# Kernel optimization log

Hardware: AMD Instinct MI355X
Metric: run time of the kernel (lower is better)

Reference implementation:

```python
import jax, jax.numpy as jnp
import numpy as np

L, B, S, D, H = 6, 2, 2048, 512, 8
DH = D // H
FF = 4 * D
EPS = 1e-5


def setup_inputs() -> dict:
    key = jax.random.key(0)
    ks = jax.random.split(key, 10)
    w = lambda k, shape: jax.random.normal(k, shape, jnp.float32) * 0.02
    return {
        "query": jax.random.normal(ks[0], (B, S, D), jnp.float32),
        "key": jax.random.normal(ks[1], (B, S, D), jnp.float32),
        "query_mask": jnp.ones((B, S), jnp.int32),
        "key_mask": jnp.ones((B, S), jnp.int32),
        # per-layer stacked params; conv1d(kernel=1) == linear with weight [out,in]
        "Wq": w(ks[2], (L, D, D)), "bq": jnp.zeros((L, D), jnp.float32),
        "Wk": w(ks[3], (L, D, D)), "bk": jnp.zeros((L, D), jnp.float32),
        "Wv": w(ks[4], (L, D, D)), "bv": jnp.zeros((L, D), jnp.float32),
        "Wo": w(ks[5], (L, D, D)), "bo": jnp.zeros((L, D), jnp.float32),
        "ln1_g": jnp.ones((L, D), jnp.float32), "ln1_b": jnp.zeros((L, D), jnp.float32),
        "ff_w1": w(ks[6], (L, FF, D)), "ff_b1": jnp.zeros((L, FF), jnp.float32),
        "ff_w2": w(ks[7], (L, D, FF)), "ff_b2": jnp.zeros((L, D), jnp.float32),
        "ln2_g": jnp.ones((L, D), jnp.float32), "ln2_b": jnp.zeros((L, D), jnp.float32),
    }


def _layer_norm(x, g, b):
    m = jnp.mean(x, axis=-1, keepdims=True)
    v = jnp.mean(jnp.square(x - m), axis=-1, keepdims=True)
    return (x - m) * jax.lax.rsqrt(v + EPS) * g + b


def reference(query, key, query_mask, key_mask,
              Wq, bq, Wk, bk, Wv, bv, Wo, bo,
              ln1_g, ln1_b, ff_w1, ff_b1, ff_w2, ff_b2, ln2_g, ln2_b):
    b_, s_, d_ = query.shape
    kpad = (key_mask == 0)[:, None, None, :]          # [B,1,1,K]
    qm = query_mask.astype(query.dtype)[:, :, None]    # [B,S,1]
    x = query
    for i in range(L):
        # QKV projections (conv1d kernel-size-1 == linear), split heads -> [B,H,S,DH]
        def split(t):
            return t.reshape(b_, s_, H, DH).transpose(0, 2, 1, 3)
        q = split(x @ Wq[i].T + bq[i]) * (float(DH) ** -0.5)
        k = split(key @ Wk[i].T + bk[i])
        v = split(key @ Wv[i].T + bv[i])
        attn = jnp.einsum('bhqd,bhkd->bhqk', q, k)
        attn = jnp.where(kpad, -jnp.inf, attn)
        attn = jax.nn.softmax(attn, axis=-1)
        o = jnp.einsum('bhqk,bhkd->bhqd', attn, v)
        o = o.transpose(0, 2, 1, 3).reshape(b_, s_, H * DH)
        o = (o @ Wo[i].T + bo[i]) * qm                 # output proj + query mask
        x = _layer_norm(o + x, ln1_g[i], ln1_b[i])
        h = jax.nn.leaky_relu(x @ ff_w1[i].T + ff_b1[i], 0.01)
        f = (h @ ff_w2[i].T + ff_b2[i]) * qm           # FFN mask on output
        x = _layer_norm(f + x, ln2_g[i], ln2_b[i])
    return x
```

## Files before the change

### kernel.cpp

```cpp
#include <hip/hip_runtime.h>
#include <stdint.h>

constexpr int LAYERS = 6;
constexpr int Bc = 2, Sc = 2048, Dc = 512, Hc = 8, DHc = 64, FFc = 2048;
constexpr int Mc = Bc * Sc;
constexpr int NS = 2;
constexpr int KCHUNK = Sc / NS;

typedef __attribute__((ext_vector_type(8))) __bf16 bf16x8;
typedef __attribute__((ext_vector_type(4))) __bf16 bf16x4;
typedef __attribute__((ext_vector_type(4))) float f32x4;

__device__ __forceinline__ void async_ld16(const void* g, void* lds) {
  __builtin_amdgcn_global_load_lds(
      (const __attribute__((address_space(1))) uint32_t*)g,
      (__attribute__((address_space(3))) uint32_t*)lds, 16, 0, 0);
}

__global__ __launch_bounds__(256) void cvt_kernel(const float* __restrict__ in,
                                                  __bf16* __restrict__ out, int n) {
  int i = (blockIdx.x * 256 + threadIdx.x) * 4;
  if (i + 4 > n) return;
  const float4 v = *(const float4*)(in + i);
  bf16x4 o;
  o[0] = (__bf16)v.x; o[1] = (__bf16)v.y; o[2] = (__bf16)v.z; o[3] = (__bf16)v.w;
  *(bf16x4*)(out + i) = o;
}

template <int BM, int BN, int WM, int WN, int EPI>
__global__ __launch_bounds__(256) void gemm_bt(
    const __bf16* __restrict__ A, const __bf16* __restrict__ W,
    const float* __restrict__ bias, const float* __restrict__ bias2,
    float* __restrict__ outf, __bf16* __restrict__ outb,
    __bf16* __restrict__ outb2, float scale,
    int M, int N, int K, int Kstride) {
  constexpr int BK = 32;
  __shared__ __bf16 As[2][BM * BK];
  __shared__ __bf16 Bs[2][BN * BK];
  const int tid = threadIdx.x;
  const int l15 = tid & 15;
  const int lg = (tid & 63) >> 4;
  const int w = tid >> 6;
  const int wm = w >> 1, wn = w & 1;
  const int tm = blockIdx.y * BM;
  const int tn = blockIdx.x * BN;
  const int z = blockIdx.z;
  const __bf16* Ap = A + (size_t)tm * Kstride + (size_t)z * K;
  const __bf16* Wp = W + (size_t)tn * Kstride + (size_t)z * K;
  f32x4 acc[WM][WN] = {};

  auto stage = [&](int k0, int bf) {
#pragma unroll
    for (int c = 0; c < BM * 4 / 256; ++c) {
      int cc = c * 256 + tid;
      async_ld16(Ap + (size_t)(cc >> 2) * Kstride + k0 + (cc & 3) * 8, &As[bf][cc * 8]);
    }
#pragma unroll
    for (int c = 0; c < BN * 4 / 256; ++c) {
      int cc = c * 256 + tid;
      async_ld16(Wp + (size_t)(cc >> 2) * Kstride + k0 + (cc & 3) * 8, &Bs[bf][cc * 8]);
    }
  };

  const int nk = K / BK;
  stage(0, 0);
  __syncthreads();
  int buf = 0;
  for (int t = 0; t < nk; ++t) {
    if (t + 1 < nk) stage((t + 1) * BK, buf ^ 1);
    bf16x8 af[WM], bfr[WN];
#pragma unroll
    for (int i = 0; i < WM; ++i)
      af[i] = *(const bf16x8*)&As[buf][(wm * WM * 16 + i * 16 + l15) * BK + lg * 8];
#pragma unroll
    for (int j = 0; j < WN; ++j)
      bfr[j] = *(const bf16x8*)&Bs[buf][(wn * WN * 16 + j * 16 + l15) * BK + lg * 8];
#pragma unroll
    for (int i = 0; i < WM; ++i)
#pragma unroll
      for (int j = 0; j < WN; ++j)
        acc[i][j] = __builtin_amdgcn_mfma_f32_16x16x32_bf16(af[i], bfr[j], acc[i][j], 0, 0, 0);
    __syncthreads();
    buf ^= 1;
  }

#pragma unroll
  for (int i = 0; i < WM; ++i) {
#pragma unroll
    for (int j = 0; j < WN; ++j) {
      const int n = tn + wn * WN * 16 + j * 16 + l15;
      float bv;
      if constexpr (EPI == 6) {
        int lyr = n >> 10, w1 = n & 1023, p = w1 >> 9, d = w1 & 511;
        bv = (p ? bias2 : bias)[lyr * 512 + d];
      } else if constexpr (EPI == 0) {
        bv = (z == 0) ? bias[n] : 0.f;
      } else {
        bv = bias[n];
      }
#pragma unroll
      for (int r = 0; r < 4; ++r) {
        const int m = tm + wm * WM * 16 + i * 16 + lg * 4 + r;
        float v = acc[i][j][r] + bv;
        if constexpr (EPI == 0) {
          outf[(size_t)z * M * N + (size_t)m * N + n] = v;
        } else if constexpr (EPI == 1) {
          int b = m >> 11, s = m & (Sc - 1);
          int h = n >> 6, dh = n & 63;
          outb[(((size_t)(b * Hc + h)) * Sc + s) * DHc + dh] = (__bf16)(v * scale);
        } else if constexpr (EPI == 4) {
          float lv = v > 0.f ? v : 0.01f * v;
          outb[(size_t)m * N + n] = (__bf16)lv;
        } else if constexpr (EPI == 6) {
          int b = m >> 11, s = m & (Sc - 1);
          int lyr = n >> 10, w1 = n & 1023, p = w1 >> 9, d = w1 & 511;
          int h = d >> 6, dh = d & 63;
          if (p == 0)
            outb[((((size_t)(lyr * Bc + b) * Hc + h)) * Sc + s) * DHc + dh] = (__bf16)v;
          else
            outb2[((((size_t)(lyr * Bc + b) * Hc + h)) * DHc + dh) * Sc + s] = (__bf16)v;
        }
      }
    }
  }
}

__global__ __launch_bounds__(256, 4) void attn_kernel(
    const __bf16* __restrict__ q, const __bf16* __restrict__ k,
    const __bf16* __restrict__ vt, const int* __restrict__ kmask,
    __bf16* __restrict__ Opart, float* __restrict__ mpart,
    float* __restrict__ lpart) {
  const int bh = blockIdx.y;
  const int b = bh >> 3;
  const int z = blockIdx.z;
  const int w = threadIdx.x >> 6;
  const int l = threadIdx.x & 63;
  const int l15 = l & 15;
  const int lg = l >> 4;
  const int tid = threadIdx.x;
  const int qbase = blockIdx.x * 64 + w * 16;
  const int k0 = z * KCHUNK;

  const __bf16* qp = q + ((size_t)bh * Sc + qbase) * DHc;
  const __bf16* kp = k + (size_t)bh * Sc * DHc;
  const __bf16* vp = vt + (size_t)bh * DHc * Sc;

  bf16x8 qf[2];
  qf[0] = *(const bf16x8*)(qp + l15 * DHc + lg * 8);
  qf[1] = *(const bf16x8*)(qp + l15 * DHc + 32 + lg * 8);

  bf16x8 onesf;
#pragma unroll
  for (int i = 0; i < 8; ++i) onesf[i] = (__bf16)1.0f;

  f32x4 oacc[4] = {};
  f32x4 lacc = {};
  float mr[4] = {-1e30f, -1e30f, -1e30f, -1e30f};

  __shared__ __bf16 Ks[2][4096];
  __shared__ __bf16 Vs[2][4096];
  __shared__ __bf16 P[4][1024];

  auto stage = [&](int t, int bf) {
    const int kt = k0 + t * 64;
#pragma unroll
    for (int ii = 0; ii < 2; ++ii) {
      int i = ii * 256 + tid;
      int r = i >> 3;
      int bsrc = (i & 7) ^ (r & 7);
      async_ld16(kp + (size_t)(kt + r) * DHc + bsrc * 8, &Ks[bf][i * 8]);
      async_ld16(vp + (size_t)r * Sc + kt + bsrc * 8, &Vs[bf][i * 8]);
    }
  };

  stage(0, 0);
  __syncthreads();

  constexpr int NT = KCHUNK / 64;
  int buf = 0;
  for (int t = 0; t < NT; ++t) {
    const int kt = k0 + t * 64;
    if (t + 1 < NT) stage(t + 1, buf ^ 1);

    f32x4 sacc[4] = {};
#pragma unroll
    for (int kf = 0; kf < 2; ++kf) {
#pragma unroll
      for (int cb = 0; cb < 4; ++cb) {
        int row = cb * 16 + l15;
        bf16x8 kfr = *(const bf16x8*)&Ks[buf][row * 64 + (((kf * 4 + lg) ^ (row & 7)) * 8)];
        sacc[cb] = __builtin_amdgcn_mfma_f32_16x16x32_bf16(qf[kf], kfr, sacc[cb], 0, 0, 0);
      }
    }
#pragma unroll
    for (int cb = 0; cb < 4; ++cb) {
      if (kmask[b * Sc + kt + cb * 16 + l15] == 0) {
        sacc[cb][0] = -1e30f; sacc[cb][1] = -1e30f;
        sacc[cb][2] = -1e30f; sacc[cb][3] = -1e30f;
      }
    }
    float mx[4];
#pragma unroll
    for (int j = 0; j < 4; ++j) {
      float m0 = fmaxf(fmaxf(sacc[0][j], sacc[1][j]), fmaxf(sacc[2][j], sacc[3][j]));
#pragma unroll
      for (int d = 1; d < 16; d <<= 1) m0 = fmaxf(m0, __shfl_xor(m0, d, 64));
      mx[j] = m0;
    }
    bool need = (mx[0] > mr[0] + 8.f) || (mx[1] > mr[1] + 8.f) ||
                (mx[2] > mr[2] + 8.f) || (mx[3] > mr[3] + 8.f);
    if (__any(need)) {
#pragma unroll
      for (int j = 0; j < 4; ++j) {
        float mn = fmaxf(mr[j], mx[j]);
        float f = __expf(mr[j] - mn);
        mr[j] = mn;
        lacc[j] *= f;
#pragma unroll
        for (int db = 0; db < 4; ++db) oacc[db][j] *= f;
      }
    }
#pragma unroll
    for (int cb = 0; cb < 4; ++cb)
#pragma unroll
      for (int j = 0; j < 4; ++j) sacc[cb][j] = __expf(sacc[cb][j] - mr[j]);

#pragma unroll
    for (int cb = 0; cb < 4; ++cb)
#pragma unroll
      for (int j = 0; j < 4; ++j) {
        int qrow = lg * 4 + j;
        P[w][qrow * 64 + ((cb * 16 + l15) ^ ((qrow & 7) << 3))] = (__bf16)sacc[cb][j];
      }
#pragma unroll
    for (int kf = 0; kf < 2; ++kf) {
      bf16x8 pf = *(const bf16x8*)&P[w][l15 * 64 + (((kf * 4 + lg) ^ (l15 & 7)) * 8)];
      lacc = __builtin_amdgcn_mfma_f32_16x16x32_bf16(pf, onesf, lacc, 0, 0, 0);
#pragma unroll
      for (int db = 0; db < 4; ++db) {
        int row = db * 16 + l15;
        bf16x8 vf = *(const bf16x8*)&Vs[buf][row * 64 + (((kf * 4 + lg) ^ (row & 7)) * 8)];
        oacc[db] = __builtin_amdgcn_mfma_f32_16x16x32_bf16(pf, vf, oacc[db], 0, 0, 0);
      }
    }
    __syncthreads();
    buf ^= 1;
  }

  const size_t obase = (((size_t)(z * Bc * Hc + bh)) * Sc + qbase) * DHc;
#pragma unroll
  for (int db = 0; db < 4; ++db)
#pragma unroll
    for (int j = 0; j < 4; ++j)
      Opart[obase + (size_t)(lg * 4 + j) * DHc + db * 16 + l15] = (__bf16)oacc[db][j];
  if (l15 == 0) {
#pragma unroll
    for (int j = 0; j < 4; ++j) {
      int row = (z * Bc * Hc + bh) * Sc + qbase + lg * 4 + j;
      mpart[row] = mr[j];
      lpart[row] = lacc[j];
    }
  }
}

__global__ __launch_bounds__(256) void attn_combine(
    const __bf16* __restrict__ Opart, const float* __restrict__ mpart,
    const float* __restrict__ lpart, __bf16* __restrict__ out) {
  int t = blockIdx.x * 256 + threadIdx.x;
  int d = t & 63;
  int row = t >> 6;
  int bh = row >> 11, s = row & (Sc - 1);
  constexpr int RSTRIDE = Bc * Hc * Sc;
  float m0 = mpart[row], m1 = mpart[RSTRIDE + row];
  float l0 = lpart[row], l1 = lpart[RSTRIDE + row];
  float M = fmaxf(m0, m1);
  float e0 = __expf(m0 - M), e1 = __expf(m1 - M);
  float denom = e0 * l0 + e1 * l1;
  float o0 = (float)Opart[(size_t)row * DHc + d];
  float o1 = (float)Opart[((size_t)RSTRIDE + row) * DHc + d];
  float o = (e0 * o0 + e1 * o1) / denom;
  int b = bh >> 3, h = bh & 7;
  out[(((size_t)b * Sc + s)) * Dc + h * DHc + d] = (__bf16)o;
}

__global__ __launch_bounds__(256) void add_ln_kernel(
    const float* __restrict__ res, const float* __restrict__ res2,
    const int* __restrict__ rmask, const float* __restrict__ xin,
    const float* __restrict__ g, const float* __restrict__ bb,
    float* __restrict__ xo, __bf16* __restrict__ xbo) {
  const int row = blockIdx.x;
  const int tid = threadIdx.x;
  const float* rp = res + (size_t)row * Dc;
  const float* xp = xin + (size_t)row * Dc;
  float mfac = rmask ? (float)rmask[row] : 1.f;
  float a0 = rp[tid], a1 = rp[tid + 256];
  if (res2) {
    const float* r2p = res2 + (size_t)row * Dc;
    a0 += r2p[tid];
    a1 += r2p[tid + 256];
  }
  float v0 = a0 * mfac + xp[tid];
  float v1 = a1 * mfac + xp[tid + 256];
  float s = v0 + v1;
#pragma unroll
  for (int d = 1; d < 64; d <<= 1) s += __shfl_xor(s, d, 64);
  __shared__ float red[4], red2[4];
  if ((tid & 63) == 0) red[tid >> 6] = s;
  __syncthreads();
  float mean = (red[0] + red[1] + red[2] + red[3]) * (1.0f / Dc);
  float d0 = v0 - mean, d1 = v1 - mean;
  float qq = d0 * d0 + d1 * d1;
#pragma unroll
  for (int d = 1; d < 64; d <<= 1) qq += __shfl_xor(qq, d, 64);
  if ((tid & 63) == 0) red2[tid >> 6] = qq;
  __syncthreads();
  float var = (red2[0] + red2[1] + red2[2] + red2[3]) * (1.0f / Dc);
  float rs = rsqrtf(var + 1e-5f);
  float o0 = d0 * rs * g[tid] + bb[tid];
  float o1 = d1 * rs * g[tid + 256] + bb[tid + 256];
  xo[(size_t)row * Dc + tid] = o0;
  xo[(size_t)row * Dc + tid + 256] = o1;
  xbo[(size_t)row * Dc + tid] = (__bf16)o0;
  xbo[(size_t)row * Dc + tid + 256] = (__bf16)o1;
}

extern "C" void kernel_launch(void* const* d_in, const int* in_sizes, int n_in,
                              void* d_out, int out_size, void* d_ws, size_t ws_size,
                              hipStream_t stream) {
  (void)in_sizes; (void)n_in; (void)out_size; (void)ws_size;
  const float* query = (const float*)d_in[0];
  const float* key   = (const float*)d_in[1];
  const int* qmask   = (const int*)d_in[2];
  const int* kmask   = (const int*)d_in[3];
  const float* Wq = (const float*)d_in[4];
  const float* bq = (const float*)d_in[5];
  const float* Wk = (const float*)d_in[6];
  const float* bk = (const float*)d_in[7];
  const float* Wv = (const float*)d_in[8];
  const float* bv = (const float*)d_in[9];
  const float* Wo = (const float*)d_in[10];
  const float* bo = (const float*)d_in[11];
  const float* ln1g = (const float*)d_in[12];
  const float* ln1b = (const float*)d_in[13];
  const float* fw1 = (const float*)d_in[14];
  const float* fb1 = (const float*)d_in[15];
  const float* fw2 = (const float*)d_in[16];
  const float* fb2 = (const float*)d_in[17];
  const float* ln2g = (const float*)d_in[18];
  const float* ln2b = (const float*)d_in[19];

  char* ws = (char*)d_ws;
  size_t off = 0;
  auto carve = [&](size_t bytes) -> void* {
    void* p = ws + off;
    off += (bytes + 255) & ~(size_t)255;
    return p;
  };
  float* x_f    = (float*)carve((size_t)Mc * Dc * 4);
  float* tmp_f  = (float*)carve((size_t)2 * Mc * Dc * 4);
  __bf16* x_b   = (__bf16*)carve((size_t)Mc * Dc * 2);
  __bf16* key_b = (__bf16*)carve((size_t)Mc * Dc * 2);
  __bf16* q_b   = (__bf16*)carve((size_t)Mc * Dc * 2);
  __bf16* at_b  = (__bf16*)carve((size_t)Mc * Dc * 2);
  __bf16* h_b   = (__bf16*)carve((size_t)Mc * FFc * 2);
  __bf16* k_all = (__bf16*)carve((size_t)LAYERS * Mc * Dc * 2);
  __bf16* vt_all= (__bf16*)carve((size_t)LAYERS * Mc * Dc * 2);
  __bf16* wq_b  = (__bf16*)carve((size_t)LAYERS * Dc * Dc * 2);
  __bf16* wkv_b = (__bf16*)carve((size_t)LAYERS * 2 * Dc * Dc * 2);
  __bf16* wo_b  = (__bf16*)carve((size_t)LAYERS * Dc * Dc * 2);
  __bf16* w1_b  = (__bf16*)carve((size_t)LAYERS * FFc * Dc * 2);
  __bf16* w2_b  = (__bf16*)carve((size_t)LAYERS * Dc * FFc * 2);
  float* ml_f   = (float*)carve((size_t)NS * Bc * Hc * Sc * 4 * 2);

  __bf16* opart_b = h_b;
  float* mpart_f = ml_f;
  float* lpart_f = ml_f + (size_t)NS * Bc * Hc * Sc;
  float* tmp2_f = tmp_f + (size_t)Mc * Dc;

  auto cvt = [&](const float* src, __bf16* dst, int n) {
    cvt_kernel<<<n / 1024, 256, 0, stream>>>(src, dst, n);
  };
  cvt(query, x_b, Mc * Dc);
  cvt(key, key_b, Mc * Dc);
  cvt(Wq, wq_b, LAYERS * Dc * Dc);
  for (int i = 0; i < LAYERS; ++i) {
    cvt(Wk + (size_t)i * Dc * Dc, wkv_b + ((size_t)i * 2 + 0) * Dc * Dc, Dc * Dc);
    cvt(Wv + (size_t)i * Dc * Dc, wkv_b + ((size_t)i * 2 + 1) * Dc * Dc, Dc * Dc);
  }
  cvt(Wo, wo_b, LAYERS * Dc * Dc);
  cvt(fw1, w1_b, LAYERS * FFc * Dc);
  cvt(fw2, w2_b, LAYERS * Dc * FFc);
  hipMemcpyAsync(x_f, query, (size_t)Mc * Dc * 4, hipMemcpyDeviceToDevice, stream);

  const dim3 blk(256);
  const dim3 gP64(Dc / 64, Mc / 64);
  const dim3 gFF2(Dc / 64, Mc / 64, 2);
  const dim3 gKV(LAYERS * 2 * Dc / 128, Mc / 128);
  const dim3 gFF1(FFc / 128, Mc / 64);
  const dim3 gAttn(Sc / 64, Bc * Hc, NS);
  const dim3 gComb(Bc * Hc * Sc * DHc / 256);

  gemm_bt<128, 128, 4, 4, 6><<<gKV, blk, 0, stream>>>(
      key_b, wkv_b, bk, bv, nullptr, k_all, vt_all, 1.0f,
      Mc, LAYERS * 2 * Dc, Dc, Dc);

  for (int i = 0; i < LAYERS; ++i) {
    const __bf16* wq_i = wq_b + (size_t)i * Dc * Dc;
    const __bf16* wo_i = wo_b + (size_t)i * Dc * Dc;
    const __bf16* w1_i = w1_b + (size_t)i * FFc * Dc;
    const __bf16* w2_i = w2_b + (size_t)i * Dc * FFc;
    const __bf16* k_i  = k_all + (size_t)i * Mc * Dc;
    const __bf16* vt_i = vt_all + (size_t)i * Mc * Dc;

    gemm_bt<64, 64, 2, 2, 1><<<gP64, blk, 0, stream>>>(
        x_b, wq_i, bq + i * Dc, nullptr, nullptr, q_b, nullptr, 0.125f,
        Mc, Dc, Dc, Dc);
    attn_kernel<<<gAttn, blk, 0, stream>>>(q_b, k_i, vt_i, kmask,
                                           opart_b, mpart_f, lpart_f);
    attn_combine<<<gComb, blk, 0, stream>>>(opart_b, mpart_f, lpart_f, at_b);
    gemm_bt<64, 64, 2, 2, 0><<<gP64, blk, 0, stream>>>(
        at_b, wo_i, bo + i * Dc, nullptr, tmp_f, nullptr, nullptr, 1.0f,
        Mc, Dc, Dc, Dc);
    add_ln_kernel<<<Mc, blk, 0, stream>>>(tmp_f, nullptr, qmask, x_f,
                                          ln1g + i * Dc, ln1b + i * Dc, x_f, x_b);
    gemm_bt<64, 128, 2, 4, 4><<<gFF1, blk, 0, stream>>>(
        x_b, w1_i, fb1 + i * FFc, nullptr, nullptr, h_b, nullptr, 1.0f,
        Mc, FFc, Dc, Dc);
    gemm_bt<64, 64, 2, 2, 0><<<gFF2, blk, 0, stream>>>(
        h_b, w2_i, fb2 + i * Dc, nullptr, tmp_f, nullptr, nullptr, 1.0f,
        Mc, Dc, FFc / 2, FFc);
    add_ln_kernel<<<Mc, blk, 0, stream>>>(tmp_f, tmp2_f, qmask, x_f,
                                          ln2g + i * Dc, ln2b + i * Dc, x_f, x_b);
  }
  hipMemcpyAsync(d_out, x_f, (size_t)Mc * Dc * 4, hipMemcpyDeviceToDevice, stream);
}
```

Measured before the change: 914.6 us.

## Widen GEMM K-tile with swizzled LDS, split-K out-proj, additive key mask

Raises the GEMM K-step from 32 to 64 and adds an XOR swizzle to the LDS layout, so each barrier covers twice the MFMA work and LDS bank conflicts drop. The output projection now uses split-K across two z-slices, and its partial sums are reduced in add_ln. Attention now adds a precomputed float mask bias with prefetching instead of branching on an int mask per tile. The twelve per-layer K/V weight conversions become one kernel, and the KV GEMM tile shrinks to 64x128. The larger tiles double LDS use per block, which can lower occupancy.

```diff
diff --git a/kernel.cpp b/kernel.cpp
--- a/kernel.cpp
+++ b/kernel.cpp
@@ -27,6 +27,26 @@
   *(bf16x4*)(out + i) = o;
 }
 
+__global__ __launch_bounds__(256) void cvt_kv_kernel(const float* __restrict__ Wk,
+                                                     const float* __restrict__ Wv,
+                                                     __bf16* __restrict__ out) {
+  size_t i = ((size_t)blockIdx.x * 256 + threadIdx.x) * 4;
+  int n = (int)(i / ((size_t)Dc * Dc));
+  int lyr = n >> 1, p = n & 1;
+  size_t idx = i - (size_t)n * Dc * Dc;
+  const float* src = (p ? Wv : Wk) + (size_t)lyr * Dc * Dc + idx;
+  const float4 v = *(const float4*)src;
+  bf16x4 o;
+  o[0] = (__bf16)v.x; o[1] = (__bf16)v.y; o[2] = (__bf16)v.z; o[3] = (__bf16)v.w;
+  *(bf16x4*)(out + i) = o;
+}
+
+__global__ __launch_bounds__(256) void kbias_kernel(const int* __restrict__ km,
+                                                    float* __restrict__ kb, int n) {
+  int i = blockIdx.x * 256 + threadIdx.x;
+  if (i < n) kb[i] = km[i] ? 0.f : -1e30f;
+}
+
 template <int BM, int BN, int WM, int WN, int EPI>
 __global__ __launch_bounds__(256) void gemm_bt(
     const __bf16* __restrict__ A, const __bf16* __restrict__ W,
@@ -34,7 +54,7 @@
     float* __restrict__ outf, __bf16* __restrict__ outb,
     __bf16* __restrict__ outb2, float scale,
     int M, int N, int K, int Kstride) {
-  constexpr int BK = 32;
+  constexpr int BK = 64;
   __shared__ __bf16 As[2][BM * BK];
   __shared__ __bf16 Bs[2][BN * BK];
   const int tid = threadIdx.x;
@@ -51,14 +71,18 @@
 
   auto stage = [&](int k0, int bf) {
 #pragma unroll
-    for (int c = 0; c < BM * 4 / 256; ++c) {
+    for (int c = 0; c < BM * 8 / 256; ++c) {
       int cc = c * 256 + tid;
-      async_ld16(Ap + (size_t)(cc >> 2) * Kstride + k0 + (cc & 3) * 8, &As[bf][cc * 8]);
-    }
-#pragma unroll
-    for (int c = 0; c < BN * 4 / 256; ++c) {
+      int r = cc >> 3, s = cc & 7;
+      int ss = s ^ (r & 7);
+      async_ld16(Ap + (size_t)r * Kstride + k0 + ss * 8, &As[bf][cc * 8]);
+    }
+#pragma unroll
+    for (int c = 0; c < BN * 8 / 256; ++c) {
       int cc = c * 256 + tid;
-      async_ld16(Wp + (size_t)(cc >> 2) * Kstride + k0 + (cc & 3) * 8, &Bs[bf][cc * 8]);
+      int r = cc >> 3, s = cc & 7;
+      int ss = s ^ (r & 7);
+      async_ld16(Wp + (size_t)r * Kstride + k0 + ss * 8, &Bs[bf][cc * 8]);
     }
   };
 
@@ -68,18 +92,28 @@
   int buf = 0;
   for (int t = 0; t < nk; ++t) {
     if (t + 1 < nk) stage((t + 1) * BK, buf ^ 1);
-    bf16x8 af[WM], bfr[WN];
-#pragma unroll
-    for (int i = 0; i < WM; ++i)
-      af[i] = *(const bf16x8*)&As[buf][(wm * WM * 16 + i * 16 + l15) * BK + lg * 8];
-#pragma unroll
-    for (int j = 0; j < WN; ++j)
-      bfr[j] = *(const bf16x8*)&Bs[buf][(wn * WN * 16 + j * 16 + l15) * BK + lg * 8];
-#pragma unroll
-    for (int i = 0; i < WM; ++i)
-#pragma unroll
-      for (int j = 0; j < WN; ++j)
-        acc[i][j] = __builtin_amdgcn_mfma_f32_16x16x32_bf16(af[i], bfr[j], acc[i][j], 0, 0, 0);
+    bf16x8 af[WM][2], bfr[WN][2];
+#pragma unroll
+    for (int i = 0; i < WM; ++i) {
+      int row = wm * WM * 16 + i * 16 + l15;
+#pragma unroll
+      for (int kf = 0; kf < 2; ++kf)
+        af[i][kf] = *(const bf16x8*)&As[buf][row * 64 + (((kf * 4 + lg) ^ (row & 7)) * 8)];
+    }
+#pragma unroll
+    for (int j = 0; j < WN; ++j) {
+      int row = wn * WN * 16 + j * 16 + l15;
+#pragma unroll
+      for (int kf = 0; kf < 2; ++kf)
+        bfr[j][kf] = *(const bf16x8*)&Bs[buf][row * 64 + (((kf * 4 + lg) ^ (row & 7)) * 8)];
+    }
+#pragma unroll
+    for (int kf = 0; kf < 2; ++kf)
+#pragma unroll
+      for (int i = 0; i < WM; ++i)
+#pragma unroll
+        for (int j = 0; j < WN; ++j)
+          acc[i][j] = __builtin_amdgcn_mfma_f32_16x16x32_bf16(af[i][kf], bfr[j][kf], acc[i][j], 0, 0, 0);
     __syncthreads();
     buf ^= 1;
   }
@@ -127,7 +161,7 @@
 
 __global__ __launch_bounds__(256, 4) void attn_kernel(
     const __bf16* __restrict__ q, const __bf16* __restrict__ k,
-    const __bf16* __restrict__ vt, const int* __restrict__ kmask,
+    const __bf16* __restrict__ vt, const float* __restrict__ kb,
     __bf16* __restrict__ Opart, float* __restrict__ mpart,
     float* __restrict__ lpart) {
   const int bh = blockIdx.y;
@@ -144,6 +178,7 @@
   const __bf16* qp = q + ((size_t)bh * Sc + qbase) * DHc;
   const __bf16* kp = k + (size_t)bh * Sc * DHc;
   const __bf16* vp = vt + (size_t)bh * DHc * Sc;
+  const float* kbp = kb + (size_t)b * Sc;
 
   bf16x8 qf[2];
   qf[0] = *(const bf16x8*)(qp + l15 * DHc + lg * 8);
@@ -173,6 +208,9 @@
     }
   };
 
+  float mb[4];
+#pragma unroll
+  for (int cb = 0; cb < 4; ++cb) mb[cb] = kbp[k0 + cb * 16 + l15];
   stage(0, 0);
   __syncthreads();
 
@@ -181,6 +219,11 @@
   for (int t = 0; t < NT; ++t) {
     const int kt = k0 + t * 64;
     if (t + 1 < NT) stage(t + 1, buf ^ 1);
+    float mbn[4];
+    if (t + 1 < NT) {
+#pragma unroll
+      for (int cb = 0; cb < 4; ++cb) mbn[cb] = kbp[kt + 64 + cb * 16 + l15];
+    }
 
     f32x4 sacc[4] = {};
 #pragma unroll
@@ -194,10 +237,8 @@
     }
 #pragma unroll
     for (int cb = 0; cb < 4; ++cb) {
-      if (kmask[b * Sc + kt + cb * 16 + l15] == 0) {
-        sacc[cb][0] = -1e30f; sacc[cb][1] = -1e30f;
-        sacc[cb][2] = -1e30f; sacc[cb][3] = -1e30f;
-      }
+#pragma unroll
+      for (int j = 0; j < 4; ++j) sacc[cb][j] += mb[cb];
     }
     float mx[4];
 #pragma unroll
@@ -242,6 +283,10 @@
         bf16x8 vf = *(const bf16x8*)&Vs[buf][row * 64 + (((kf * 4 + lg) ^ (row & 7)) * 8)];
         oacc[db] = __builtin_amdgcn_mfma_f32_16x16x32_bf16(pf, vf, oacc[db], 0, 0, 0);
       }
+    }
+    if (t + 1 < NT) {
+#pragma unroll
+      for (int cb = 0; cb < 4; ++cb) mb[cb] = mbn[cb];
     }
     __syncthreads();
     buf ^= 1;
@@ -371,6 +416,7 @@
   __bf16* w1_b  = (__bf16*)carve((size_t)LAYERS * FFc * Dc * 2);
   __bf16* w2_b  = (__bf16*)carve((size_t)LAYERS * Dc * FFc * 2);
   float* ml_f   = (float*)carve((size_t)NS * Bc * Hc * Sc * 4 * 2);
+  float* kb_f   = (float*)carve((size_t)Bc * Sc * 4);
 
   __bf16* opart_b = h_b;
   float* mpart_f = ml_f;
@@ -383,24 +429,23 @@
   cvt(query, x_b, Mc * Dc);
   cvt(key, key_b, Mc * Dc);
   cvt(Wq, wq_b, LAYERS * Dc * Dc);
-  for (int i = 0; i < LAYERS; ++i) {
-    cvt(Wk + (size_t)i * Dc * Dc, wkv_b + ((size_t)i * 2 + 0) * Dc * Dc, Dc * Dc);
-    cvt(Wv + (size_t)i * Dc * Dc, wkv_b + ((size_t)i * 2 + 1) * Dc * Dc, Dc * Dc);
-  }
+  cvt_kv_kernel<<<LAYERS * 2 * Dc * Dc / 1024, 256, 0, stream>>>(Wk, Wv, wkv_b);
   cvt(Wo, wo_b, LAYERS * Dc * Dc);
   cvt(fw1, w1_b, LAYERS * FFc * Dc);
   cvt(fw2, w2_b, LAYERS * Dc * FFc);
+  kbias_kernel<<<Bc * Sc / 256, 256, 0, stream>>>(kmask, kb_f, Bc * Sc);
   hipMemcpyAsync(x_f, query, (size_t)Mc * Dc * 4, hipMemcpyDeviceToDevice, stream);
 
   const dim3 blk(256);
   const dim3 gP64(Dc / 64, Mc / 64);
+  const dim3 gOP(Dc / 64, Mc / 64, 2);
   const dim3 gFF2(Dc / 64, Mc / 64, 2);
-  const dim3 gKV(LAYERS * 2 * Dc / 128, Mc / 128);
+  const dim3 gKV(LAYERS * 2 * Dc / 128, Mc / 64);
   const dim3 gFF1(FFc / 128, Mc / 64);
   const dim3 gAttn(Sc / 64, Bc * Hc, NS);
   const dim3 gComb(Bc * Hc * Sc * DHc / 256);
 
-  gemm_bt<128, 128, 4, 4, 6><<<gKV, blk, 0, stream>>>(
+  gemm_bt<64, 128, 2, 4, 6><<<gKV, blk, 0, stream>>>(
       key_b, wkv_b, bk, bv, nullptr, k_all, vt_all, 1.0f,
       Mc, LAYERS * 2 * Dc, Dc, Dc);
 
@@ -415,13 +460,13 @@
     gemm_bt<64, 64, 2, 2, 1><<<gP64, blk, 0, stream>>>(
         x_b, wq_i, bq + i * Dc, nullptr, nullptr, q_b, nullptr, 0.125f,
         Mc, Dc, Dc, Dc);
-    attn_kernel<<<gAttn, blk, 0, stream>>>(q_b, k_i, vt_i, kmask,
+    attn_kernel<<<gAttn, blk, 0, stream>>>(q_b, k_i, vt_i, kb_f,
                                            opart_b, mpart_f, lpart_f);
     attn_combine<<<gComb, blk, 0, stream>>>(opart_b, mpart_f, lpart_f, at_b);
-    gemm_bt<64, 64, 2, 2, 0><<<gP64, blk, 0, stream>>>(
+    gemm_bt<64, 64, 2, 2, 0><<<gOP, blk, 0, stream>>>(
         at_b, wo_i, bo + i * Dc, nullptr, tmp_f, nullptr, nullptr, 1.0f,
-        Mc, Dc, Dc, Dc);
-    add_ln_kernel<<<Mc, blk, 0, stream>>>(tmp_f, nullptr, qmask, x_f,
+        Mc, Dc, Dc / 2, Dc);
+    add_ln_kernel<<<Mc, blk, 0, stream>>>(tmp_f, tmp2_f, qmask, x_f,
                                           ln1g + i * Dc, ln1b + i * Dc, x_f, x_b);
     gemm_bt<64, 128, 2, 4, 4><<<gFF1, blk, 0, stream>>>(
         x_b, w1_i, fb1 + i * FFc, nullptr, nullptr, h_b, nullptr, 1.0f,
```

New measurement: 876.1 us. -4.2%, faster.
